# Performance work log

Measured on AMD Instinct MI355X. Metric: run time of the kernel, lower is better.

Reference implementation:

```python
import jax, jax.numpy as jnp
import numpy as np

B, S, D = 4, 2048, 1024
NH, HD = 16, 64  # num_heads, head_dim; NH*HD == D


def setup_inputs() -> dict:
    key = jax.random.key(0)
    ks = jax.random.split(key, 10)
    s = 0.02
    return {
        "x": jax.random.normal(ks[0], (B, S, D), dtype=jnp.float32),
        "attention_mask": jnp.zeros((B, 1, 1, S), dtype=jnp.float32),
        "Wq": jax.random.normal(ks[1], (D, D), dtype=jnp.float32) * s,
        "bq": jnp.zeros((D,), dtype=jnp.float32),
        "Wk": jax.random.normal(ks[2], (D, D), dtype=jnp.float32) * s,
        "bk": jnp.zeros((D,), dtype=jnp.float32),
        "Wv": jax.random.normal(ks[3], (D, D), dtype=jnp.float32) * s,
        "bv": jnp.zeros((D,), dtype=jnp.float32),
        "Wo": jax.random.normal(ks[4], (D, D), dtype=jnp.float32) * s,
        "bo": jnp.zeros((D,), dtype=jnp.float32),
    }


def _heads(t):
    # [B,S,D] -> [B,NH,S,HD]
    return t.reshape(B, S, NH, HD).transpose(0, 2, 1, 3)


def reference(x, attention_mask, Wq, bq, Wk, bk, Wv, bv, Wo, bo):
    q = _heads(x @ Wq + bq)
    k = _heads(x @ Wk + bk)
    v = _heads(x @ Wv + bv)
    scores = jnp.einsum("bhqd,bhkd->bhqk", q, k) / jnp.sqrt(jnp.float32(HD))
    scores = scores + attention_mask
    attn = jax.nn.softmax(scores, axis=-1)  # dropout p=0 -> identity
    ctx = jnp.einsum("bhqk,bhkd->bhqd", attn, v)
    ctx = ctx.transpose(0, 2, 1, 3).reshape(B, S, D)
    return ctx @ Wo + bo
```

## Files before the change

kernel.cpp:

```cpp
#include <hip/hip_runtime.h>
#include <cstdint>
#include <cstddef>

typedef unsigned short u16;
typedef __attribute__((ext_vector_type(8))) __bf16 bf16x8;
typedef __attribute__((ext_vector_type(4))) float f32x4;
typedef __attribute__((ext_vector_type(16))) float f32x16;
typedef __attribute__((ext_vector_type(2))) uint32_t u32x2;
typedef __attribute__((ext_vector_type(4))) float float4v;

#define BATCH 4
#define S_LEN 2048
#define DMODEL 1024
#define NHEAD 16
#define HDIM 64
#define MROWS (BATCH * S_LEN)
#define LOG2E 1.4426950408889634f
#define SC_L (0.125f * LOG2E)

__device__ __forceinline__ u16 f2bf(float f) {
  uint32_t u = __float_as_uint(f);
  u += 0x7fffu + ((u >> 16) & 1u);
  return (u16)(u >> 16);
}

#if __has_builtin(__builtin_amdgcn_cvt_pk_bf16_f32)
__device__ __forceinline__ uint32_t packbf2(float a, float b) {
  auto t = __builtin_amdgcn_cvt_pk_bf16_f32(a, b);
  uint32_t u;
  __builtin_memcpy(&u, &t, 4);
  return u;
}
#else
__device__ __forceinline__ uint32_t packbf2(float a, float b) {
  uint32_t ua = __float_as_uint(a) + 0x8000u;
  uint32_t ub = __float_as_uint(b) + 0x8000u;
  return (ub & 0xFFFF0000u) | (ua >> 16);
}
#endif

#if __has_builtin(__builtin_amdgcn_exp2f)
#define EXP2(x) __builtin_amdgcn_exp2f(x)
#else
#define EXP2(x) exp2f(x)
#endif

typedef __attribute__((address_space(1))) void gvoid_t;
typedef __attribute__((address_space(3))) void svoid_t;
__device__ __forceinline__ void gl_lds16(const void* g, void* s) {
  __builtin_amdgcn_global_load_lds((gvoid_t*)g, (svoid_t*)s, 16, 0, 0);
}

__global__ __launch_bounds__(256) void cvt4_kernel(const float4v* __restrict__ in,
                                                   u32x2* __restrict__ out, int n4) {
  int i = blockIdx.x * blockDim.x + threadIdx.x;
  if (i < n4) {
    float4v v = in[i];
    u32x2 o;
    o.x = packbf2(v.x, v.y);
    o.y = packbf2(v.z, v.w);
    out[i] = o;
  }
}

__global__ __launch_bounds__(256) void maskl_kernel(const float* __restrict__ in,
                                                    float* __restrict__ out, int n) {
  int i = blockIdx.x * blockDim.x + threadIdx.x;
  if (i < n) out[i] = in[i] * LOG2E;
}

__global__ __launch_bounds__(256) void tcvt_kernel(const float* __restrict__ W0,
                                                   const float* __restrict__ W1,
                                                   const float* __restrict__ W2,
                                                   const float* __restrict__ W3,
                                                   u16* __restrict__ Wall) {
  __shared__ float tile[32][33];
  const int z = blockIdx.z;
  const float* W = (z == 0) ? W0 : (z == 1) ? W1 : (z == 2) ? W2 : W3;
  u16* Wt = Wall + (size_t)z * DMODEL * DMODEL;
  const int n0 = blockIdx.x * 32, k0 = blockIdx.y * 32;
  const int x = threadIdx.x, y = threadIdx.y;
  for (int yy = y; yy < 32; yy += 8)
    tile[yy][x] = W[(size_t)(k0 + yy) * DMODEL + n0 + x];
  __syncthreads();
  for (int yy = y; yy < 32; yy += 8)
    Wt[(size_t)(n0 + yy) * DMODEL + k0 + x] = f2bf(tile[x][yy]);
}

template <int MODE>
__global__ __launch_bounds__(256) void gemm128(const u16* __restrict__ A,
                                               const u16* __restrict__ Bt,
                                               const float* __restrict__ b0,
                                               const float* __restrict__ b1,
                                               const float* __restrict__ b2,
                                               void* __restrict__ o0,
                                               void* __restrict__ o1,
                                               void* __restrict__ o2) {
  __shared__ u16 As[128 * 32];
  __shared__ u16 Bs[128 * 32];
  const int tid = threadIdx.x;
  const int wid = tid >> 6;
  const int lane = tid & 63;
  const int l16 = lane & 15;
  const int g4 = lane >> 4;
  const int m0 = blockIdx.x * 128;
  const int n0 = blockIdx.y * 128;
  const int wm = (wid & 1) * 64;
  const int wn = (wid >> 1) * 64;

  const int srow = tid >> 2;
  const int sk = (tid & 3) * 8;
  const u16* gA = A + (size_t)(m0 + srow) * DMODEL + sk;
  const u16* gB = Bt + (size_t)(n0 + srow) * DMODEL + sk;
  char* sA = (char*)As + wid * 1024;
  char* sB = (char*)Bs + wid * 1024;

  f32x4 acc[4][4];
#pragma unroll
  for (int i = 0; i < 4; ++i)
#pragma unroll
    for (int j = 0; j < 4; ++j) acc[i][j] = (f32x4){0.f, 0.f, 0.f, 0.f};

  for (int k0 = 0; k0 < DMODEL; k0 += 32) {
    __syncthreads();
    gl_lds16(gA + k0, sA);
    gl_lds16(gA + (size_t)64 * DMODEL + k0, sA + 4096);
    gl_lds16(gB + k0, sB);
    gl_lds16(gB + (size_t)64 * DMODEL + k0, sB + 4096);
    __syncthreads();

    bf16x8 af[4], bfr[4];
#pragma unroll
    for (int i = 0; i < 4; ++i)
      af[i] = *(const bf16x8*)(As + (wm + i * 16 + l16) * 32 + g4 * 8);
#pragma unroll
    for (int j = 0; j < 4; ++j)
      bfr[j] = *(const bf16x8*)(Bs + (wn + j * 16 + l16) * 32 + g4 * 8);
#pragma unroll
    for (int i = 0; i < 4; ++i)
#pragma unroll
      for (int j = 0; j < 4; ++j)
        acc[i][j] = __builtin_amdgcn_mfma_f32_16x16x32_bf16(af[i], bfr[j],
                                                            acc[i][j], 0, 0, 0);
  }

  const int seg = n0 >> 10;
  const float* bp = (MODE == 1 || seg == 0) ? b0 : (seg == 1 ? b1 : b2);
  void* op = (MODE == 1 || seg == 0) ? o0 : (seg == 1 ? o1 : o2);

#pragma unroll
  for (int i = 0; i < 4; ++i) {
#pragma unroll
    for (int j = 0; j < 4; ++j) {
      const int coll = n0 + wn + j * 16 + l16;
      const int cseg = coll & 1023;
      const float bval = bp[cseg];
#pragma unroll
      for (int r = 0; r < 4; ++r) {
        const int rowg = m0 + wm + i * 16 + g4 * 4 + r;
        const float v = acc[i][j][r] + bval;
        if (MODE == 0) {
          const int b = rowg >> 11, s = rowg & (S_LEN - 1);
          const int h = cseg >> 6, d = cseg & (HDIM - 1);
          if (seg == 2) {
            ((u16*)op)[(((size_t)(b * NHEAD + h) * HDIM + d) << 11) + s] = f2bf(v);
          } else {
            ((u16*)op)[((size_t)((b * NHEAD + h) * S_LEN + s) << 6) + d] = f2bf(v);
          }
        } else {
          ((float*)op)[(size_t)rowg * DMODEL + cseg] = v;
        }
      }
    }
  }
}

__global__ __launch_bounds__(256, 2) void attn4_kernel(const u16* __restrict__ Q,
                                                       const u16* __restrict__ K,
                                                       const u16* __restrict__ Vt,
                                                       const float* __restrict__ maskL,
                                                       u16* __restrict__ ctx) {
  __shared__ u16 Ks[64 * 72];
  __shared__ u16 Vs[64 * 72];

  const int tid = threadIdx.x;
  const int wid = tid >> 6;
  const int lane = tid & 63;
  const int l32 = lane & 31;
  const int hi = lane >> 5;
  const int flat = blockIdx.y * gridDim.x + blockIdx.x;
  const int nf = (flat & 7) * 64 + (flat >> 3);
  const int bx = nf & 7;
  const int bh = nf >> 3;
  const int b = bh >> 4;
  const int h = bh & 15;
  const int qw0 = bx * 256 + wid * 64;

  const u16* Qbase = Q + (size_t)bh * S_LEN * HDIM;
  bf16x8 aq[2][4];
#pragma unroll
  for (int qh = 0; qh < 2; ++qh)
#pragma unroll
    for (int c = 0; c < 4; ++c)
      aq[qh][c] = *(const bf16x8*)(Qbase + (size_t)(qw0 + qh * 32 + l32) * HDIM +
                                   c * 16 + hi * 8);

  union { u16 s[8]; bf16x8 v; } onesu;
#pragma unroll
  for (int i = 0; i < 8; ++i) onesu.s[i] = 0x3F80;
  const bf16x8 onesv = onesu.v;

  const f32x16 z16 = {};
  f32x16 oacc[2][2] = {};
  f32x16 lacc[2] = {};

  const int srow = tid >> 3;
  const int scol = (tid & 7) * 8;
  const int keyg = scol >> 4;
  const int todd = (scol >> 3) & 1;
  const int vkb = keyg * 16 + todd * 4;
  const u16* Kg = K + (size_t)bh * S_LEN * HDIM + (size_t)srow * HDIM + scol;
  const u16* Vg = Vt + (size_t)bh * HDIM * S_LEN + (size_t)srow * S_LEN + scol;
  const float* mrow = maskL + (size_t)b * S_LEN;

  for (int kt = 0; kt < S_LEN; kt += 64) {
    bf16x8 kv0 = *(const bf16x8*)(Kg + (size_t)kt * HDIM);
    bf16x8 kv1 = *(const bf16x8*)(Kg + (size_t)(kt + 32) * HDIM);
    union { bf16x8 v; uint32_t u[4]; } vv0, vv1;
    vv0.v = *(const bf16x8*)(Vg + kt);
    vv1.v = *(const bf16x8*)(Vg + (size_t)32 * S_LEN + kt);
    __syncthreads();
    *(bf16x8*)(Ks + srow * 72 + scol) = kv0;
    *(bf16x8*)(Ks + (srow + 32) * 72 + scol) = kv1;
    *(u32x2*)(Vs + srow * 72 + vkb) = (u32x2){vv0.u[0], vv0.u[1]};
    *(u32x2*)(Vs + srow * 72 + vkb + 8) = (u32x2){vv0.u[2], vv0.u[3]};
    *(u32x2*)(Vs + (srow + 32) * 72 + vkb) = (u32x2){vv1.u[0], vv1.u[1]};
    *(u32x2*)(Vs + (srow + 32) * 72 + vkb + 8) = (u32x2){vv1.u[2], vv1.u[3]};
    __syncthreads();

    uint32_t P[2][2][8];
#pragma unroll
    for (int T = 0; T < 2; ++T) {
      bf16x8 kf[4];
#pragma unroll
      for (int c = 0; c < 4; ++c)
        kf[c] = *(const bf16x8*)(Ks + (T * 32 + l32) * 72 + c * 16 + hi * 8);
      f32x4 m4[4];
#pragma unroll
      for (int tq = 0; tq < 4; ++tq)
        m4[tq] = *(const f32x4*)(mrow + kt + T * 32 + tq * 8 + hi * 4);
#pragma unroll
      for (int qh = 0; qh < 2; ++qh) {
        f32x16 s = __builtin_amdgcn_mfma_f32_32x32x16_bf16(kf[0], aq[qh][0], z16, 0, 0, 0);
#pragma unroll
        for (int c = 1; c < 4; ++c)
          s = __builtin_amdgcn_mfma_f32_32x32x16_bf16(kf[c], aq[qh][c], s, 0, 0, 0);
#pragma unroll
        for (int tq = 0; tq < 4; ++tq) {
          float p0 = EXP2(fmaf(s[tq * 4 + 0], SC_L, m4[tq][0]));
          float p1 = EXP2(fmaf(s[tq * 4 + 1], SC_L, m4[tq][1]));
          float p2 = EXP2(fmaf(s[tq * 4 + 2], SC_L, m4[tq][2]));
          float p3 = EXP2(fmaf(s[tq * 4 + 3], SC_L, m4[tq][3]));
          P[T][qh][tq * 2] = packbf2(p0, p1);
          P[T][qh][tq * 2 + 1] = packbf2(p2, p3);
        }
      }
    }

#pragma unroll
    for (int c = 0; c < 4; ++c) {
      const int T = c >> 1, half = c & 1;
      bf16x8 vf[2];
#pragma unroll
      for (int dh = 0; dh < 2; ++dh)
        vf[dh] = *(const bf16x8*)(Vs + (dh * 32 + l32) * 72 + c * 16 + hi * 8);
#pragma unroll
      for (int qh = 0; qh < 2; ++qh) {
        union { uint32_t u[4]; bf16x8 v; } pf;
#pragma unroll
        for (int e = 0; e < 4; ++e) pf.u[e] = P[T][qh][half * 4 + e];
        oacc[qh][0] = __builtin_amdgcn_mfma_f32_32x32x16_bf16(pf.v, vf[0], oacc[qh][0], 0, 0, 0);
        oacc[qh][1] = __builtin_amdgcn_mfma_f32_32x32x16_bf16(pf.v, vf[1], oacc[qh][1], 0, 0, 0);
        lacc[qh] = __builtin_amdgcn_mfma_f32_32x32x16_bf16(pf.v, onesv, lacc[qh], 0, 0, 0);
      }
    }
  }

#pragma unroll
  for (int qh = 0; qh < 2; ++qh) {
#pragma unroll
    for (int reg = 0; reg < 16; ++reg) {
      const int q = qw0 + qh * 32 + (reg & 3) + 8 * (reg >> 2) + 4 * hi;
      const float inv = 1.0f / lacc[qh][reg];
      u16* cp = ctx + ((size_t)(b * S_LEN + q) * NHEAD + h) * HDIM;
      cp[l32] = f2bf(oacc[qh][0][reg] * inv);
      cp[32 + l32] = f2bf(oacc[qh][1][reg] * inv);
    }
  }
}

extern "C" void kernel_launch(void* const* d_in, const int* in_sizes, int n_in,
                              void* d_out, int out_size, void* d_ws, size_t ws_size,
                              hipStream_t stream) {
  const float* x = (const float*)d_in[0];
  const float* mask = (const float*)d_in[1];
  const float* Wq = (const float*)d_in[2];
  const float* bq = (const float*)d_in[3];
  const float* Wk = (const float*)d_in[4];
  const float* bk = (const float*)d_in[5];
  const float* Wv = (const float*)d_in[6];
  const float* bv = (const float*)d_in[7];
  const float* Wo = (const float*)d_in[8];
  const float* bo = (const float*)d_in[9];
  float* out = (float*)d_out;

  char* ws = (char*)d_ws;
  size_t off = 0;
  u16* xb = (u16*)(ws + off);    off += (size_t)MROWS * DMODEL * 2;
  u16* wall = (u16*)(ws + off);  off += (size_t)4 * DMODEL * DMODEL * 2;
  u16* Qh = (u16*)(ws + off);    off += (size_t)MROWS * DMODEL * 2;
  u16* Kh = (u16*)(ws + off);    off += (size_t)MROWS * DMODEL * 2;
  u16* Vtb = (u16*)(ws + off);   off += (size_t)MROWS * DMODEL * 2;
  u16* ctxb = (u16*)(ws + off);  off += (size_t)MROWS * DMODEL * 2;
  float* mL = (float*)(ws + off); off += (size_t)BATCH * S_LEN * 4;
  (void)ws_size; (void)in_sizes; (void)n_in; (void)out_size;

  const int nx4 = MROWS * DMODEL / 4;
  cvt4_kernel<<<dim3(nx4 / 256), dim3(256), 0, stream>>>((const float4v*)x, (u32x2*)xb, nx4);
  maskl_kernel<<<dim3(BATCH * S_LEN / 256), dim3(256), 0, stream>>>(mask, mL, BATCH * S_LEN);
  tcvt_kernel<<<dim3(32, 32, 4), dim3(32, 8), 0, stream>>>(Wq, Wk, Wv, Wo, wall);

  gemm128<0><<<dim3(MROWS / 128, 3 * DMODEL / 128), dim3(256), 0, stream>>>(
      xb, wall, bq, bk, bv, (void*)Qh, (void*)Kh, (void*)Vtb);

  attn4_kernel<<<dim3(S_LEN / 256, BATCH * NHEAD), dim3(256), 0, stream>>>(Qh, Kh, Vtb, mL, ctxb);

  gemm128<1><<<dim3(MROWS / 128, DMODEL / 128), dim3(256), 0, stream>>>(
      ctxb, wall + (size_t)3 * DMODEL * DMODEL, bo, bo, bo, (void*)out, (void*)out, (void*)out);
}
```

Measured before the change: 296.9 us.

## Double-buffer K/V tiles in attention, add MFMA priority, and swizzle GEMM block order

The attention kernel now uses two LDS buffers for K/V tiles. It prefetches the next tile's global loads before computing on the current one, so each iteration needs one barrier instead of two and memory latency overlaps with compute. MFMA sections are wrapped in s_setprio to favour matrix issue. The GEMM remaps its flat block index into 8 interleaved groups to change cache locality. The costs are more LDS (which may hurt the 2-blocks-per-CU occupancy target) and more live registers. The GEMM remap hardcodes 64 M-blocks.

```diff
diff --git a/kernel.cpp b/kernel.cpp
--- a/kernel.cpp
+++ b/kernel.cpp
@@ -103,8 +103,11 @@
   const int lane = tid & 63;
   const int l16 = lane & 15;
   const int g4 = lane >> 4;
-  const int m0 = blockIdx.x * 128;
-  const int n0 = blockIdx.y * 128;
+  const int nwg = gridDim.x * gridDim.y;
+  int flat = blockIdx.y * gridDim.x + blockIdx.x;
+  flat = (flat & 7) * (nwg >> 3) + (flat >> 3);
+  const int m0 = (flat & 63) * 128;
+  const int n0 = (flat >> 6) * 128;
   const int wm = (wid & 1) * 64;
   const int wn = (wid >> 1) * 64;
 
@@ -180,8 +183,8 @@
                                                        const u16* __restrict__ Vt,
                                                        const float* __restrict__ maskL,
                                                        u16* __restrict__ ctx) {
-  __shared__ u16 Ks[64 * 72];
-  __shared__ u16 Vs[64 * 72];
+  __shared__ u16 Ks[2][64 * 72];
+  __shared__ u16 Vs[2][64 * 72];
 
   const int tid = threadIdx.x;
   const int wid = tid >> 6;
@@ -223,38 +226,49 @@
   const u16* Vg = Vt + (size_t)bh * HDIM * S_LEN + (size_t)srow * S_LEN + scol;
   const float* mrow = maskL + (size_t)b * S_LEN;
 
-  for (int kt = 0; kt < S_LEN; kt += 64) {
-    bf16x8 kv0 = *(const bf16x8*)(Kg + (size_t)kt * HDIM);
-    bf16x8 kv1 = *(const bf16x8*)(Kg + (size_t)(kt + 32) * HDIM);
-    union { bf16x8 v; uint32_t u[4]; } vv0, vv1;
+  bf16x8 kv0, kv1;
+  union VU { bf16x8 v; uint32_t u[4]; };
+  VU vv0, vv1;
+
+  auto LOADT = [&](int kt) {
+    kv0 = *(const bf16x8*)(Kg + (size_t)kt * HDIM);
+    kv1 = *(const bf16x8*)(Kg + (size_t)(kt + 32) * HDIM);
     vv0.v = *(const bf16x8*)(Vg + kt);
     vv1.v = *(const bf16x8*)(Vg + (size_t)32 * S_LEN + kt);
-    __syncthreads();
-    *(bf16x8*)(Ks + srow * 72 + scol) = kv0;
-    *(bf16x8*)(Ks + (srow + 32) * 72 + scol) = kv1;
-    *(u32x2*)(Vs + srow * 72 + vkb) = (u32x2){vv0.u[0], vv0.u[1]};
-    *(u32x2*)(Vs + srow * 72 + vkb + 8) = (u32x2){vv0.u[2], vv0.u[3]};
-    *(u32x2*)(Vs + (srow + 32) * 72 + vkb) = (u32x2){vv1.u[0], vv1.u[1]};
-    *(u32x2*)(Vs + (srow + 32) * 72 + vkb + 8) = (u32x2){vv1.u[2], vv1.u[3]};
-    __syncthreads();
-
+  };
+  auto STORET = [&](int buf) {
+    u16* Kb = &Ks[buf][0];
+    u16* Vb = &Vs[buf][0];
+    *(bf16x8*)(Kb + srow * 72 + scol) = kv0;
+    *(bf16x8*)(Kb + (srow + 32) * 72 + scol) = kv1;
+    *(u32x2*)(Vb + srow * 72 + vkb) = (u32x2){vv0.u[0], vv0.u[1]};
+    *(u32x2*)(Vb + srow * 72 + vkb + 8) = (u32x2){vv0.u[2], vv0.u[3]};
+    *(u32x2*)(Vb + (srow + 32) * 72 + vkb) = (u32x2){vv1.u[0], vv1.u[1]};
+    *(u32x2*)(Vb + (srow + 32) * 72 + vkb + 8) = (u32x2){vv1.u[2], vv1.u[3]};
+  };
+
+  auto COMPUTE = [&](int buf, int kt) {
+    const u16* Kb = &Ks[buf][0];
+    const u16* Vb = &Vs[buf][0];
     uint32_t P[2][2][8];
 #pragma unroll
     for (int T = 0; T < 2; ++T) {
       bf16x8 kf[4];
 #pragma unroll
       for (int c = 0; c < 4; ++c)
-        kf[c] = *(const bf16x8*)(Ks + (T * 32 + l32) * 72 + c * 16 + hi * 8);
+        kf[c] = *(const bf16x8*)(Kb + (T * 32 + l32) * 72 + c * 16 + hi * 8);
       f32x4 m4[4];
 #pragma unroll
       for (int tq = 0; tq < 4; ++tq)
         m4[tq] = *(const f32x4*)(mrow + kt + T * 32 + tq * 8 + hi * 4);
 #pragma unroll
       for (int qh = 0; qh < 2; ++qh) {
+        __builtin_amdgcn_s_setprio(1);
         f32x16 s = __builtin_amdgcn_mfma_f32_32x32x16_bf16(kf[0], aq[qh][0], z16, 0, 0, 0);
 #pragma unroll
         for (int c = 1; c < 4; ++c)
           s = __builtin_amdgcn_mfma_f32_32x32x16_bf16(kf[c], aq[qh][c], s, 0, 0, 0);
+        __builtin_amdgcn_s_setprio(0);
 #pragma unroll
         for (int tq = 0; tq < 4; ++tq) {
           float p0 = EXP2(fmaf(s[tq * 4 + 0], SC_L, m4[tq][0]));
@@ -273,7 +287,8 @@
       bf16x8 vf[2];
 #pragma unroll
       for (int dh = 0; dh < 2; ++dh)
-        vf[dh] = *(const bf16x8*)(Vs + (dh * 32 + l32) * 72 + c * 16 + hi * 8);
+        vf[dh] = *(const bf16x8*)(Vb + (dh * 32 + l32) * 72 + c * 16 + hi * 8);
+      __builtin_amdgcn_s_setprio(1);
 #pragma unroll
       for (int qh = 0; qh < 2; ++qh) {
         union { uint32_t u[4]; bf16x8 v; } pf;
@@ -283,8 +298,22 @@
         oacc[qh][1] = __builtin_amdgcn_mfma_f32_32x32x16_bf16(pf.v, vf[1], oacc[qh][1], 0, 0, 0);
         lacc[qh] = __builtin_amdgcn_mfma_f32_32x32x16_bf16(pf.v, onesv, lacc[qh], 0, 0, 0);
       }
+      __builtin_amdgcn_s_setprio(0);
     }
-  }
+  };
+
+  LOADT(0);
+  STORET(0);
+  __syncthreads();
+  int cur = 0;
+  for (int kt = 0; kt < S_LEN - 64; kt += 64) {
+    LOADT(kt + 64);
+    COMPUTE(cur, kt);
+    STORET(cur ^ 1);
+    __syncthreads();
+    cur ^= 1;
+  }
+  COMPUTE(cur, S_LEN - 64);
 
 #pragma unroll
   for (int qh = 0; qh < 2; ++qh) {
```

After: 325.5 us. 1.1x slower.
